# Kernel optimization log

Hardware: AMD Instinct MI355X
Metric: run time of the kernel (lower is better)

The kernel has to match this reference:

```python
import jax, jax.numpy as jnp
import numpy as np

ALPHA_MEM = 0.95      # util.decayconst(tau_mem)
ALPHA_MEM_OUT = 0.95  # util.decayconst(tau_mem_out)
ALPHA_P = 0.99        # util.decayconst(tau_p)
SURR_SCALE = 100.0

@jax.custom_vjp
def spike(x):
    # Heaviside forward, surrogate gradient backward (SurrGradSpike)
    return (x > 0).astype(x.dtype)

def _spike_fwd(x):
    return spike(x), x

def _spike_bwd(x, g):
    return (g / (SURR_SCALE * jnp.abs(x) + 1.0) ** 2,)

spike.defvjp(_spike_fwd, _spike_bwd)


def setup_inputs() -> dict:
    B, T, N, NIN, NOUT, D = 64, 400, 1024, 128, 32, 3
    key = jax.random.key(0)
    ks = jax.random.split(key, 8)
    inputs = jax.random.normal(ks[0], (B, T, NIN), dtype=jnp.float32)
    w = jax.random.normal(ks[1], (N, N), dtype=jnp.float32) / np.sqrt(N).astype(np.float32)
    w_in = jax.random.normal(ks[2], (NIN, N), dtype=jnp.float32) * np.float32(0.3 / np.sqrt(NIN))
    w_out = jax.random.normal(ks[3], (N, NOUT), dtype=jnp.float32) * np.float32(0.3 / np.sqrt(N))
    w_signs = jnp.where(jax.random.uniform(ks[4], (N,)) < 0.8, 1.0, -1.0).astype(jnp.float32)
    dmap = (jax.random.uniform(ks[5], (D, N, N)) < 0.2).astype(jnp.float32)  # delay-wise connectivity mask
    p = jax.random.uniform(ks[6], (N,), minval=-0.5, maxval=0.5).astype(jnp.float32)
    delays = jnp.array([1, 2, 4], dtype=jnp.int32)
    return dict(inputs=inputs, w=w, w_in=w_in, w_out=w_out, w_signs=w_signs,
                dmap=dmap, p=p, delays=delays)


def _forward(inputs, w, w_in, w_out, w_signs, dmap, p, delays):
    B, T, _ = inputs.shape
    N = w.shape[0]
    L = int(np.max(np.asarray(delays))) + 1  # ring-buffer length (static)
    dtype = inputs.dtype

    inp = jnp.einsum('btc,cn->btn', inputs, w_in)           # epoch.input, (B,T,N)
    W = dmap * (w_signs[:, None] * jnp.abs(w))[None]        # (D,N,N)
    depr = (p < 0).astype(dtype)                            # p_depr_mask

    def step(carry, inp_t):
        mem, w_p, buf_out, buf_wp, t = carry
        out = spike(mem - 1.0)                              # mark_spikes
        buf_out = buf_out.at[t % L].set(out)                # record_state
        buf_wp = buf_wp.at[t % L].set(w_p)
        idx = (t - delays) % L
        syn_p = buf_out[idx] * (1.0 + buf_wp[idx])          # (D,B,N)
        syn = jnp.einsum('dbe,deo->bo', syn_p, W)
        w_p_new = w_p * ALPHA_P + out * p * (1.0 + depr * w_p)
        mem_new = ALPHA_MEM * mem + inp_t + syn - jax.lax.stop_gradient(out)
        return (mem_new, w_p_new, buf_out, buf_wp, t + 1), out

    z = jnp.zeros((B, N), dtype)
    bufs = jnp.zeros((L, B, N), dtype)
    carry0 = (z, z, bufs, bufs, jnp.int32(0))
    _, out_rec = jax.lax.scan(step, carry0, jnp.swapaxes(inp, 0, 1))  # (T,B,N)

    # compute_readout: leaky integrator over projected spikes
    h2 = jnp.einsum('tbn,no->tbo', out_rec, w_out)
    def ro_step(r, h):
        r = ALPHA_MEM_OUT * r + h
        return r, r
    _, readout = jax.lax.scan(ro_step, jnp.zeros((B, w_out.shape[1]), dtype), h2)
    return jnp.swapaxes(readout, 0, 1)                      # (B,T,NOUT)


def reference(inputs, w, w_in, w_out, w_signs, dmap, p, delays):
    return _forward(inputs, w, w_in, w_out, w_signs, dmap, p, delays)
```

## Files before the change

### kernel.cpp

```cpp
#include <hip/hip_runtime.h>
#include <cstdint>
#include <cstddef>

#define BB    64
#define TT    400
#define NN    1024
#define NIN   128
#define NOUT  32
#define DD    3
#define LL6   6
#define GG    16
#define BPG   4
#define NT    32
#define KK    3072

#define ALPHA_MEM     0.95f
#define ALPHA_MEM_OUT 0.95f
#define ALPHA_P       0.99f

__global__ void build_W(const float* __restrict__ w,
                        const float* __restrict__ w_signs,
                        const float* __restrict__ dmap,
                        float* __restrict__ W) {
    int idx = blockIdx.x * blockDim.x + threadIdx.x;
    if (idx >= DD * NN * NN) return;
    int en = idx % (NN * NN);
    int e  = en / NN;
    W[idx] = dmap[idx] * (w_signs[e] * fabsf(w[en]));
}

__global__ void gemm_in(const float* __restrict__ inputs,
                        const float* __restrict__ w_in,
                        float* __restrict__ inp) {
    int idx = blockIdx.x * blockDim.x + threadIdx.x;
    if (idx >= TT * BB * NN) return;
    int n  = idx & (NN - 1);
    int tb = idx >> 10;
    int b  = tb & 63;
    int t  = tb >> 6;
    const float* row = inputs + ((size_t)b * TT + t) * NIN;
    float acc = 0.0f;
    #pragma unroll 8
    for (int c = 0; c < NIN; ++c)
        acc = fmaf(row[c], w_in[c * NN + n], acc);
    inp[idx] = acc;
}

__global__ void zero_sc1(float* __restrict__ p, int n) {
    int i = blockIdx.x * blockDim.x + threadIdx.x;
    if (i < n)
        __hip_atomic_store(p + i, 0.0f, __ATOMIC_RELAXED, __HIP_MEMORY_SCOPE_AGENT);
}

__global__ __launch_bounds__(256, 2) void snn_scan(
    const float* __restrict__ inputs,
    const float* __restrict__ w_in,
    const float* __restrict__ w_out,
    const float* __restrict__ p,
    const int*   __restrict__ delays,
    const float* __restrict__ W,
    const float* __restrict__ w_raw,
    const float* __restrict__ w_signs,
    const float* __restrict__ dmap,
    float*       __restrict__ ring,
    int*         __restrict__ cnt,
    float*       __restrict__ hpart,
    const float* __restrict__ inp_pre,
    float*       __restrict__ out,
    int use_pre, int use_W)
{
    __shared__ __align__(16) float sa[KK * BPG];
    __shared__ float w_out_s[32 * NOUT];
    __shared__ float spk_s[BPG * 32];
    __shared__ float s_sign[NN];
    __shared__ float s_in[BPG * NIN];

    const int bid  = blockIdx.x;
    const int g    = bid >> 5;
    const int tile = bid & 31;
    const int tid  = threadIdx.x;
    const int lane = tid & 63;
    const int wv   = tid >> 6;

    const bool st = (tid < BPG * 32);
    const int  sb = tid >> 5;
    const int  nl = tid & 31;

    const int gks = tid >> 3;
    const int gcg = tid & 7;

    float mem = 0.0f, wp = 0.0f, r = 0.0f;
    float pn = 0.0f, depr = 0.0f;
    if (st) { pn = p[tile * 32 + nl]; depr = (pn < 0.0f) ? 1.0f : 0.0f; }

    const int d0 = delays[0], d1 = delays[1], d2 = delays[2];

    for (int k = tid; k < 32 * NOUT; k += 256)
        w_out_s[k] = w_out[(tile * 32 + (k >> 5)) * NOUT + (k & 31)];
    if (!use_W)
        for (int k = tid; k < NN; k += 256) s_sign[k] = w_signs[k];
    __syncthreads();

    const float* Wt = W     + tile * 32 + gcg * 4;
    const float* Dt = dmap  + tile * 32 + gcg * 4;
    const float* Rt = w_raw + tile * 32 + gcg * 4;

    for (int t = 0; t < TT; ++t) {
        const int slot_w = t % LL6;
        const int s0 = (t - d0 + 2 * LL6) % LL6;
        const int s1 = (t - d1 + 2 * LL6) % LL6;
        const int s2 = (t - d2 + 2 * LL6) % LL6;

        bool  spk = false;
        float ia  = 0.0f;
        if (st) {
            spk = (mem - 1.0f) > 0.0f;
            const float a = spk ? (1.0f + wp) : 0.0f;
            __hip_atomic_store(ring + (((size_t)slot_w * BB + g * BPG + sb) << 10)
                                    + tile * 32 + nl,
                               a, __ATOMIC_RELAXED, __HIP_MEMORY_SCOPE_AGENT);
            wp = ALPHA_P * wp + (spk ? pn * (1.0f + depr * wp) : 0.0f);
            spk_s[tid] = spk ? 1.0f : 0.0f;
            if (use_pre)
                ia = inp_pre[((size_t)t * BB + g * BPG + sb) * NN + tile * 32 + nl];
        }
        if (!use_pre) {
            for (int k = tid; k < BPG * NIN; k += 256) {
                int b2 = k >> 7, c = k & 127;
                s_in[k] = inputs[((size_t)(g * BPG + b2) * TT + t) * NIN + c];
            }
        }
        __syncthreads();

        if (st) {
            float h = 0.0f;
            #pragma unroll
            for (int n2 = 0; n2 < 32; ++n2)
                h = fmaf(spk_s[sb * 32 + n2], w_out_s[n2 * 32 + nl], h);
            __hip_atomic_store(hpart + ((((size_t)(t & 1) * NT + tile) * BB)
                                        + g * BPG + sb) * NOUT + nl,
                               h, __ATOMIC_RELAXED, __HIP_MEMORY_SCOPE_AGENT);
            if (!use_pre) {
                #pragma unroll 8
                for (int c = 0; c < NIN; ++c)
                    ia = fmaf(s_in[sb * NIN + c], w_in[c * NN + tile * 32 + nl], ia);
            }
        }
        __syncthreads();

        if (tid == 0)
            __hip_atomic_fetch_add(&cnt[g * 32], 1, __ATOMIC_RELEASE,
                                   __HIP_MEMORY_SCOPE_AGENT);

        {
            const int b2 = lane >> 4;
            const int eo = lane & 15;
            #pragma unroll 16
            for (int i = 0; i < 48; ++i) {
                const int c  = i * 4 + wv;
                const int kl = c * 16 + eo;
                const int d  = kl >> 10;
                const int e  = kl & 1023;
                const int sl = (d == 0) ? s0 : ((d == 1) ? s1 : s2);
                const float v = __hip_atomic_load(
                    ring + (((size_t)sl * BB + g * BPG + b2) << 10) + e,
                    __ATOMIC_RELAXED, __HIP_MEMORY_SCOPE_AGENT);
                sa[kl * 4 + b2] = v;
            }
        }
        __syncthreads();

        if (tid == 0) {
            const int target = 32 * (t + 1);
            while (__hip_atomic_load(&cnt[g * 32], __ATOMIC_ACQUIRE,
                                     __HIP_MEMORY_SCOPE_AGENT) < target)
                __builtin_amdgcn_s_sleep(2);
        }
        __syncthreads();

        if (tile == 0 && st) {
            float h = 0.0f;
            #pragma unroll
            for (int k3 = 0; k3 < NT; ++k3)
                h += __hip_atomic_load(hpart + ((((size_t)(t & 1) * NT + k3) * BB)
                                                + g * BPG + sb) * NOUT + nl,
                                       __ATOMIC_RELAXED, __HIP_MEMORY_SCOPE_AGENT);
            r = ALPHA_MEM_OUT * r + h;
            out[((size_t)(g * BPG + sb) * TT + t) * NOUT + nl] = r;
        }

        float4 acc0 = {0,0,0,0}, acc1 = {0,0,0,0}, acc2 = {0,0,0,0}, acc3 = {0,0,0,0};
        if (use_W) {
            #pragma unroll 8
            for (int i = 0; i < 96; ++i) {
                const int kk = gks + (i << 5);
                const float4 av = *(const float4*)&sa[kk << 2];
                const float4 wv4 = *(const float4*)(Wt + ((size_t)kk << 10));
                acc0.x = fmaf(av.x, wv4.x, acc0.x); acc0.y = fmaf(av.x, wv4.y, acc0.y);
                acc0.z = fmaf(av.x, wv4.z, acc0.z); acc0.w = fmaf(av.x, wv4.w, acc0.w);
                acc1.x = fmaf(av.y, wv4.x, acc1.x); acc1.y = fmaf(av.y, wv4.y, acc1.y);
                acc1.z = fmaf(av.y, wv4.z, acc1.z); acc1.w = fmaf(av.y, wv4.w, acc1.w);
                acc2.x = fmaf(av.z, wv4.x, acc2.x); acc2.y = fmaf(av.z, wv4.y, acc2.y);
                acc2.z = fmaf(av.z, wv4.z, acc2.z); acc2.w = fmaf(av.z, wv4.w, acc2.w);
                acc3.x = fmaf(av.w, wv4.x, acc3.x); acc3.y = fmaf(av.w, wv4.y, acc3.y);
                acc3.z = fmaf(av.w, wv4.z, acc3.z); acc3.w = fmaf(av.w, wv4.w, acc3.w);
            }
        } else {
            #pragma unroll 2
            for (int i = 0; i < 96; ++i) {
                const int kk = gks + (i << 5);
                const int e  = kk & 1023;
                const float sg = s_sign[e];
                const float4 dm = *(const float4*)(Dt + ((size_t)kk << 10));
                const float4 wr = *(const float4*)(Rt + ((size_t)e << 10));
                float4 wv4;
                wv4.x = dm.x * (sg * fabsf(wr.x));
                wv4.y = dm.y * (sg * fabsf(wr.y));
                wv4.z = dm.z * (sg * fabsf(wr.z));
                wv4.w = dm.w * (sg * fabsf(wr.w));
                const float4 av = *(const float4*)&sa[kk << 2];
                acc0.x = fmaf(av.x, wv4.x, acc0.x); acc0.y = fmaf(av.x, wv4.y, acc0.y);
                acc0.z = fmaf(av.x, wv4.z, acc0.z); acc0.w = fmaf(av.x, wv4.w, acc0.w);
                acc1.x = fmaf(av.y, wv4.x, acc1.x); acc1.y = fmaf(av.y, wv4.y, acc1.y);
                acc1.z = fmaf(av.y, wv4.z, acc1.z); acc1.w = fmaf(av.y, wv4.w, acc1.w);
                acc2.x = fmaf(av.z, wv4.x, acc2.x); acc2.y = fmaf(av.z, wv4.y, acc2.y);
                acc2.z = fmaf(av.z, wv4.z, acc2.z); acc2.w = fmaf(av.z, wv4.w, acc2.w);
                acc3.x = fmaf(av.w, wv4.x, acc3.x); acc3.y = fmaf(av.w, wv4.y, acc3.y);
                acc3.z = fmaf(av.w, wv4.z, acc3.z); acc3.w = fmaf(av.w, wv4.w, acc3.w);
            }
        }
        __syncthreads();

        float* red = sa;
        {
            const int o0 = gcg * 4;
            red[(0 * 32 + o0 + 0) * 33 + gks] = acc0.x;
            red[(0 * 32 + o0 + 1) * 33 + gks] = acc0.y;
            red[(0 * 32 + o0 + 2) * 33 + gks] = acc0.z;
            red[(0 * 32 + o0 + 3) * 33 + gks] = acc0.w;
            red[(1 * 32 + o0 + 0) * 33 + gks] = acc1.x;
            red[(1 * 32 + o0 + 1) * 33 + gks] = acc1.y;
            red[(1 * 32 + o0 + 2) * 33 + gks] = acc1.z;
            red[(1 * 32 + o0 + 3) * 33 + gks] = acc1.w;
            red[(2 * 32 + o0 + 0) * 33 + gks] = acc2.x;
            red[(2 * 32 + o0 + 1) * 33 + gks] = acc2.y;
            red[(2 * 32 + o0 + 2) * 33 + gks] = acc2.z;
            red[(2 * 32 + o0 + 3) * 33 + gks] = acc2.w;
            red[(3 * 32 + o0 + 0) * 33 + gks] = acc3.x;
            red[(3 * 32 + o0 + 1) * 33 + gks] = acc3.y;
            red[(3 * 32 + o0 + 2) * 33 + gks] = acc3.z;
            red[(3 * 32 + o0 + 3) * 33 + gks] = acc3.w;
        }
        __syncthreads();

        if (st) {
            float syn = 0.0f;
            #pragma unroll
            for (int k2 = 0; k2 < 32; ++k2)
                syn += red[tid * 33 + k2];
            mem = ALPHA_MEM * mem + ia + syn - (spk ? 1.0f : 0.0f);
        }
        __syncthreads();
    }
}

extern "C" void kernel_launch(void* const* d_in, const int* in_sizes, int n_in,
                              void* d_out, int out_size, void* d_ws, size_t ws_size,
                              hipStream_t stream) {
    const float* inputs  = (const float*)d_in[0];
    const float* w       = (const float*)d_in[1];
    const float* w_in    = (const float*)d_in[2];
    const float* w_out   = (const float*)d_in[3];
    const float* w_signs = (const float*)d_in[4];
    const float* dmap    = (const float*)d_in[5];
    const float* p       = (const float*)d_in[6];
    const int*   delays  = (const int*)d_in[7];
    float*       outp    = (float*)d_out;

    const size_t ring_f = (size_t)LL6 * BB * NN;
    const size_t cnt_f  = GG * 32;
    const size_t hp_f   = (size_t)2 * NT * BB * NOUT;
    const size_t W_f    = (size_t)DD * NN * NN;
    const size_t pre_f  = (size_t)TT * BB * NN;

    float* ws = (float*)d_ws;
    float* ring  = ws;
    int*   cntp  = (int*)(ws + ring_f);
    float* hpart = ws + ring_f + cnt_f;
    size_t used  = ring_f + cnt_f + hp_f;

    int use_W = 0, use_pre = 0;
    float *W = nullptr, *inp_pre = nullptr;
    if (ws_size >= (used + W_f) * 4)   { use_W = 1;   W = ws + used;       used += W_f; }
    if (ws_size >= (used + pre_f) * 4) { use_pre = 1; inp_pre = ws + used; used += pre_f; }

    if (use_W) {
        const int total = DD * NN * NN;
        build_W<<<(total + 255) / 256, 256, 0, stream>>>(w, w_signs, dmap, W);
    }
    if (use_pre) {
        const int total = TT * BB * NN;
        gemm_in<<<(total + 255) / 256, 256, 0, stream>>>(inputs, w_in, inp_pre);
    }
    {
        const int total = (int)(ring_f + cnt_f);
        zero_sc1<<<(total + 255) / 256, 256, 0, stream>>>(ring, total);
    }

    void* args[] = {
        (void*)&inputs, (void*)&w_in, (void*)&w_out, (void*)&p, (void*)&delays,
        (void*)&W, (void*)&w, (void*)&w_signs, (void*)&dmap,
        (void*)&ring, (void*)&cntp, (void*)&hpart, (void*)&inp_pre, (void*)&outp,
        (void*)&use_pre, (void*)&use_W
    };
    hipError_t cerr = hipLaunchCooperativeKernel((const void*)snn_scan,
                               dim3(GG * NT), dim3(256), args, 0, stream);
    if (cerr != hipSuccess) {
        hipLaunchKernelGGL(snn_scan, dim3(GG * NT), dim3(256), 0, stream,
                           inputs, w_in, w_out, p, delays, W, w, w_signs, dmap,
                           ring, cntp, hpart, inp_pre, outp, use_pre, use_W);
    }
}
```

Baseline: 11.38 ms.

## Pack masked recurrent weights into fixed-capacity per-column sparse lists

A new pre-pass kernel builds, for each output neuron, a padded list of (row index, value) pairs holding the nonzero entries of the masked delay-stacked weight matrix, capped at 800 entries. The recurrent step then gathers spike activations from shared memory by index and multiplies only by the nonzero weights. The dense 3072-row sweep is kept as a fallback. The goal is to cut per-step weight traffic and FMAs by exploiting the roughly 20% connectivity density. In exchange, shared-memory reads become irregular gathers that can hit bank conflicts, and any column with more than 800 nonzeros is silently truncated.

```diff
diff --git a/kernel.cpp b/kernel.cpp
--- a/kernel.cpp
+++ b/kernel.cpp
@@ -13,6 +13,7 @@
 #define BPG   4
 #define NT    32
 #define KK    3072
+#define CAP   800
 
 #define ALPHA_MEM     0.95f
 #define ALPHA_MEM_OUT 0.95f
@@ -27,6 +28,42 @@
     int en = idx % (NN * NN);
     int e  = en / NN;
     W[idx] = dmap[idx] * (w_signs[e] * fabsf(w[en]));
+}
+
+__global__ void build_csr(const float* __restrict__ W,
+                          uint2* __restrict__ pack) {
+    const int col = blockIdx.x;
+    const int tid = threadIdx.x;
+    __shared__ int pref[256];
+    __shared__ int total_s;
+
+    int cnt = 0;
+    #pragma unroll
+    for (int i = 0; i < 12; ++i) {
+        const float v = W[(size_t)(tid * 12 + i) * NN + col];
+        cnt += (v != 0.0f) ? 1 : 0;
+    }
+    pref[tid] = cnt;
+    __syncthreads();
+    if (tid == 0) {
+        int run = 0;
+        for (int j = 0; j < 256; ++j) { int c = pref[j]; pref[j] = run; run += c; }
+        total_s = run;
+    }
+    __syncthreads();
+
+    int ofs = pref[tid];
+    #pragma unroll
+    for (int i = 0; i < 12; ++i) {
+        const int k = tid * 12 + i;
+        const float v = W[(size_t)k * NN + col];
+        if (v != 0.0f && ofs < CAP) {
+            pack[(size_t)col * CAP + ofs] = make_uint2((unsigned)k, __float_as_uint(v));
+            ++ofs;
+        }
+    }
+    for (int s = total_s + tid; s < CAP; s += 256)
+        pack[(size_t)col * CAP + s] = make_uint2(0u, 0u);
 }
 
 __global__ void gemm_in(const float* __restrict__ inputs,
@@ -66,8 +103,9 @@
     int*         __restrict__ cnt,
     float*       __restrict__ hpart,
     const float* __restrict__ inp_pre,
+    const uint2* __restrict__ pack,
     float*       __restrict__ out,
-    int use_pre, int use_W)
+    int use_pre, int use_W, int use_csr)
 {
     __shared__ __align__(16) float sa[KK * BPG];
     __shared__ float w_out_s[32 * NOUT];
@@ -89,6 +127,9 @@
     const int gks = tid >> 3;
     const int gcg = tid & 7;
 
+    const int colg = tid >> 3;
+    const int sub  = tid & 7;
+
     float mem = 0.0f, wp = 0.0f, r = 0.0f;
     float pn = 0.0f, depr = 0.0f;
     if (st) { pn = p[tile * 32 + nl]; depr = (pn < 0.0f) ? 1.0f : 0.0f; }
@@ -104,6 +145,7 @@
     const float* Wt = W     + tile * 32 + gcg * 4;
     const float* Dt = dmap  + tile * 32 + gcg * 4;
     const float* Rt = w_raw + tile * 32 + gcg * 4;
+    const uint2* Pk = pack  + (size_t)(tile * 32 + colg) * CAP;
 
     for (int t = 0; t < TT; ++t) {
         const int slot_w = t % LL6;
@@ -189,78 +231,109 @@
             out[((size_t)(g * BPG + sb) * TT + t) * NOUT + nl] = r;
         }
 
-        float4 acc0 = {0,0,0,0}, acc1 = {0,0,0,0}, acc2 = {0,0,0,0}, acc3 = {0,0,0,0};
-        if (use_W) {
-            #pragma unroll 8
-            for (int i = 0; i < 96; ++i) {
-                const int kk = gks + (i << 5);
-                const float4 av = *(const float4*)&sa[kk << 2];
-                const float4 wv4 = *(const float4*)(Wt + ((size_t)kk << 10));
-                acc0.x = fmaf(av.x, wv4.x, acc0.x); acc0.y = fmaf(av.x, wv4.y, acc0.y);
-                acc0.z = fmaf(av.x, wv4.z, acc0.z); acc0.w = fmaf(av.x, wv4.w, acc0.w);
-                acc1.x = fmaf(av.y, wv4.x, acc1.x); acc1.y = fmaf(av.y, wv4.y, acc1.y);
-                acc1.z = fmaf(av.y, wv4.z, acc1.z); acc1.w = fmaf(av.y, wv4.w, acc1.w);
-                acc2.x = fmaf(av.z, wv4.x, acc2.x); acc2.y = fmaf(av.z, wv4.y, acc2.y);
-                acc2.z = fmaf(av.z, wv4.z, acc2.z); acc2.w = fmaf(av.z, wv4.w, acc2.w);
-                acc3.x = fmaf(av.w, wv4.x, acc3.x); acc3.y = fmaf(av.w, wv4.y, acc3.y);
-                acc3.z = fmaf(av.w, wv4.z, acc3.z); acc3.w = fmaf(av.w, wv4.w, acc3.w);
-            }
+        if (use_csr) {
+            float a0 = 0.0f, a1 = 0.0f, a2 = 0.0f, a3 = 0.0f;
+            #pragma unroll 4
+            for (int i = 0; i < CAP / 8; ++i) {
+                const uint2 pv = Pk[i * 8 + sub];
+                const float v  = __uint_as_float(pv.y);
+                const float4 av = *(const float4*)&sa[pv.x << 2];
+                a0 = fmaf(av.x, v, a0);
+                a1 = fmaf(av.y, v, a1);
+                a2 = fmaf(av.z, v, a2);
+                a3 = fmaf(av.w, v, a3);
+            }
+            __syncthreads();
+
+            float* red = sa;
+            red[(colg * 4 + 0) * 9 + sub] = a0;
+            red[(colg * 4 + 1) * 9 + sub] = a1;
+            red[(colg * 4 + 2) * 9 + sub] = a2;
+            red[(colg * 4 + 3) * 9 + sub] = a3;
+            __syncthreads();
+
+            if (st) {
+                float syn = 0.0f;
+                #pragma unroll
+                for (int k2 = 0; k2 < 8; ++k2)
+                    syn += red[(nl * 4 + sb) * 9 + k2];
+                mem = ALPHA_MEM * mem + ia + syn - (spk ? 1.0f : 0.0f);
+            }
+            __syncthreads();
         } else {
-            #pragma unroll 2
-            for (int i = 0; i < 96; ++i) {
-                const int kk = gks + (i << 5);
-                const int e  = kk & 1023;
-                const float sg = s_sign[e];
-                const float4 dm = *(const float4*)(Dt + ((size_t)kk << 10));
-                const float4 wr = *(const float4*)(Rt + ((size_t)e << 10));
-                float4 wv4;
-                wv4.x = dm.x * (sg * fabsf(wr.x));
-                wv4.y = dm.y * (sg * fabsf(wr.y));
-                wv4.z = dm.z * (sg * fabsf(wr.z));
-                wv4.w = dm.w * (sg * fabsf(wr.w));
-                const float4 av = *(const float4*)&sa[kk << 2];
-                acc0.x = fmaf(av.x, wv4.x, acc0.x); acc0.y = fmaf(av.x, wv4.y, acc0.y);
-                acc0.z = fmaf(av.x, wv4.z, acc0.z); acc0.w = fmaf(av.x, wv4.w, acc0.w);
-                acc1.x = fmaf(av.y, wv4.x, acc1.x); acc1.y = fmaf(av.y, wv4.y, acc1.y);
-                acc1.z = fmaf(av.y, wv4.z, acc1.z); acc1.w = fmaf(av.y, wv4.w, acc1.w);
-                acc2.x = fmaf(av.z, wv4.x, acc2.x); acc2.y = fmaf(av.z, wv4.y, acc2.y);
-                acc2.z = fmaf(av.z, wv4.z, acc2.z); acc2.w = fmaf(av.z, wv4.w, acc2.w);
-                acc3.x = fmaf(av.w, wv4.x, acc3.x); acc3.y = fmaf(av.w, wv4.y, acc3.y);
-                acc3.z = fmaf(av.w, wv4.z, acc3.z); acc3.w = fmaf(av.w, wv4.w, acc3.w);
-            }
-        }
-        __syncthreads();
-
-        float* red = sa;
-        {
-            const int o0 = gcg * 4;
-            red[(0 * 32 + o0 + 0) * 33 + gks] = acc0.x;
-            red[(0 * 32 + o0 + 1) * 33 + gks] = acc0.y;
-            red[(0 * 32 + o0 + 2) * 33 + gks] = acc0.z;
-            red[(0 * 32 + o0 + 3) * 33 + gks] = acc0.w;
-            red[(1 * 32 + o0 + 0) * 33 + gks] = acc1.x;
-            red[(1 * 32 + o0 + 1) * 33 + gks] = acc1.y;
-            red[(1 * 32 + o0 + 2) * 33 + gks] = acc1.z;
-            red[(1 * 32 + o0 + 3) * 33 + gks] = acc1.w;
-            red[(2 * 32 + o0 + 0) * 33 + gks] = acc2.x;
-            red[(2 * 32 + o0 + 1) * 33 + gks] = acc2.y;
-            red[(2 * 32 + o0 + 2) * 33 + gks] = acc2.z;
-            red[(2 * 32 + o0 + 3) * 33 + gks] = acc2.w;
-            red[(3 * 32 + o0 + 0) * 33 + gks] = acc3.x;
-            red[(3 * 32 + o0 + 1) * 33 + gks] = acc3.y;
-            red[(3 * 32 + o0 + 2) * 33 + gks] = acc3.z;
-            red[(3 * 32 + o0 + 3) * 33 + gks] = acc3.w;
-        }
-        __syncthreads();
-
-        if (st) {
-            float syn = 0.0f;
-            #pragma unroll
-            for (int k2 = 0; k2 < 32; ++k2)
-                syn += red[tid * 33 + k2];
-            mem = ALPHA_MEM * mem + ia + syn - (spk ? 1.0f : 0.0f);
-        }
-        __syncthreads();
+            float4 acc0 = {0,0,0,0}, acc1 = {0,0,0,0}, acc2 = {0,0,0,0}, acc3 = {0,0,0,0};
+            if (use_W) {
+                #pragma unroll 8
+                for (int i = 0; i < 96; ++i) {
+                    const int kk = gks + (i << 5);
+                    const float4 av = *(const float4*)&sa[kk << 2];
+                    const float4 wv4 = *(const float4*)(Wt + ((size_t)kk << 10));
+                    acc0.x = fmaf(av.x, wv4.x, acc0.x); acc0.y = fmaf(av.x, wv4.y, acc0.y);
+                    acc0.z = fmaf(av.x, wv4.z, acc0.z); acc0.w = fmaf(av.x, wv4.w, acc0.w);
+                    acc1.x = fmaf(av.y, wv4.x, acc1.x); acc1.y = fmaf(av.y, wv4.y, acc1.y);
+                    acc1.z = fmaf(av.y, wv4.z, acc1.z); acc1.w = fmaf(av.y, wv4.w, acc1.w);
+                    acc2.x = fmaf(av.z, wv4.x, acc2.x); acc2.y = fmaf(av.z, wv4.y, acc2.y);
+                    acc2.z = fmaf(av.z, wv4.z, acc2.z); acc2.w = fmaf(av.z, wv4.w, acc2.w);
+                    acc3.x = fmaf(av.w, wv4.x, acc3.x); acc3.y = fmaf(av.w, wv4.y, acc3.y);
+                    acc3.z = fmaf(av.w, wv4.z, acc3.z); acc3.w = fmaf(av.w, wv4.w, acc3.w);
+                }
+            } else {
+                #pragma unroll 2
+                for (int i = 0; i < 96; ++i) {
+                    const int kk = gks + (i << 5);
+                    const int e  = kk & 1023;
+                    const float sg = s_sign[e];
+                    const float4 dm = *(const float4*)(Dt + ((size_t)kk << 10));
+                    const float4 wr = *(const float4*)(Rt + ((size_t)e << 10));
+                    float4 wv4;
+                    wv4.x = dm.x * (sg * fabsf(wr.x));
+                    wv4.y = dm.y * (sg * fabsf(wr.y));
+                    wv4.z = dm.z * (sg * fabsf(wr.z));
+                    wv4.w = dm.w * (sg * fabsf(wr.w));
+                    const float4 av = *(const float4*)&sa[kk << 2];
+                    acc0.x = fmaf(av.x, wv4.x, acc0.x); acc0.y = fmaf(av.x, wv4.y, acc0.y);
+                    acc0.z = fmaf(av.x, wv4.z, acc0.z); acc0.w = fmaf(av.x, wv4.w, acc0.w);
+                    acc1.x = fmaf(av.y, wv4.x, acc1.x); acc1.y = fmaf(av.y, wv4.y, acc1.y);
+                    acc1.z = fmaf(av.y, wv4.z, acc1.z); acc1.w = fmaf(av.y, wv4.w, acc1.w);
+                    acc2.x = fmaf(av.z, wv4.x, acc2.x); acc2.y = fmaf(av.z, wv4.y, acc2.y);
+                    acc2.z = fmaf(av.z, wv4.z, acc2.z); acc2.w = fmaf(av.z, wv4.w, acc2.w);
+                    acc3.x = fmaf(av.w, wv4.x, acc3.x); acc3.y = fmaf(av.w, wv4.y, acc3.y);
+                    acc3.z = fmaf(av.w, wv4.z, acc3.z); acc3.w = fmaf(av.w, wv4.w, acc3.w);
+                }
+            }
+            __syncthreads();
+
+            float* red = sa;
+            {
+                const int o0 = gcg * 4;
+                red[(0 * 32 + o0 + 0) * 33 + gks] = acc0.x;
+                red[(0 * 32 + o0 + 1) * 33 + gks] = acc0.y;
+                red[(0 * 32 + o0 + 2) * 33 + gks] = acc0.z;
+                red[(0 * 32 + o0 + 3) * 33 + gks] = acc0.w;
+                red[(1 * 32 + o0 + 0) * 33 + gks] = acc1.x;
+                red[(1 * 32 + o0 + 1) * 33 + gks] = acc1.y;
+                red[(1 * 32 + o0 + 2) * 33 + gks] = acc1.z;
+                red[(1 * 32 + o0 + 3) * 33 + gks] = acc1.w;
+                red[(2 * 32 + o0 + 0) * 33 + gks] = acc2.x;
+                red[(2 * 32 + o0 + 1) * 33 + gks] = acc2.y;
+                red[(2 * 32 + o0 + 2) * 33 + gks] = acc2.z;
+                red[(2 * 32 + o0 + 3) * 33 + gks] = acc2.w;
+                red[(3 * 32 + o0 + 0) * 33 + gks] = acc3.x;
+                red[(3 * 32 + o0 + 1) * 33 + gks] = acc3.y;
+                red[(3 * 32 + o0 + 2) * 33 + gks] = acc3.z;
+                red[(3 * 32 + o0 + 3) * 33 + gks] = acc3.w;
+            }
+            __syncthreads();
+
+            if (st) {
+                float syn = 0.0f;
+                #pragma unroll
+                for (int k2 = 0; k2 < 32; ++k2)
+                    syn += red[tid * 33 + k2];
+                mem = ALPHA_MEM * mem + ia + syn - (spk ? 1.0f : 0.0f);
+            }
+            __syncthreads();
+        }
     }
 }
 
@@ -282,6 +355,7 @@
     const size_t hp_f   = (size_t)2 * NT * BB * NOUT;
     const size_t W_f    = (size_t)DD * NN * NN;
     const size_t pre_f  = (size_t)TT * BB * NN;
+    const size_t csr_f  = (size_t)NN * CAP * 2;
 
     float* ws = (float*)d_ws;
     float* ring  = ws;
@@ -289,15 +363,21 @@
     float* hpart = ws + ring_f + cnt_f;
     size_t used  = ring_f + cnt_f + hp_f;
 
-    int use_W = 0, use_pre = 0;
+    int use_W = 0, use_pre = 0, use_csr = 0;
     float *W = nullptr, *inp_pre = nullptr;
+    uint2 *pack = nullptr;
     if (ws_size >= (used + W_f) * 4)   { use_W = 1;   W = ws + used;       used += W_f; }
     if (ws_size >= (used + pre_f) * 4) { use_pre = 1; inp_pre = ws + used; used += pre_f; }
+    if (use_W && ws_size >= (used + csr_f) * 4) {
+        use_csr = 1; pack = (uint2*)(ws + used); used += csr_f;
+    }
 
     if (use_W) {
         const int total = DD * NN * NN;
         build_W<<<(total + 255) / 256, 256, 0, stream>>>(w, w_signs, dmap, W);
     }
+    if (use_csr)
+        build_csr<<<NN, 256, 0, stream>>>(W, pack);
     if (use_pre) {
         const int total = TT * BB * NN;
         gemm_in<<<(total + 255) / 256, 256, 0, stream>>>(inputs, w_in, inp_pre);
@@ -310,14 +390,15 @@
     void* args[] = {
         (void*)&inputs, (void*)&w_in, (void*)&w_out, (void*)&p, (void*)&delays,
         (void*)&W, (void*)&w, (void*)&w_signs, (void*)&dmap,
-        (void*)&ring, (void*)&cntp, (void*)&hpart, (void*)&inp_pre, (void*)&outp,
-        (void*)&use_pre, (void*)&use_W
+        (void*)&ring, (void*)&cntp, (void*)&hpart, (void*)&inp_pre, (void*)&pack,
+        (void*)&outp, (void*)&use_pre, (void*)&use_W, (void*)&use_csr
     };
     hipError_t cerr = hipLaunchCooperativeKernel((const void*)snn_scan,
                                dim3(GG * NT), dim3(256), args, 0, stream);
     if (cerr != hipSuccess) {
         hipLaunchKernelGGL(snn_scan, dim3(GG * NT), dim3(256), 0, stream,
                            inputs, w_in, w_out, p, delays, W, w, w_signs, dmap,
-                           ring, cntp, hpart, inp_pre, outp, use_pre, use_W);
-    }
-}
+                           ring, cntp, hpart, inp_pre, pack, outp,
+                           use_pre, use_W, use_csr);
+    }
+}
```

Result: faster. 10.95 ms (-3.8%).

## Gather only nonzero delayed spikes into per-wave active lists for synaptic sums

Applied to the files above, without the earlier changes.

Each wave now owns one batch row. It uses a ballot and popcount to compact the nonzero delayed presynaptic activations into an LDS list of (index, value) pairs. The synaptic sum then gathers only the W rows for those active entries, with two half-waves splitting the list and combining through a shuffle. This replaces the dense 3072-row accumulation, the LDS reduction and several block barriers, so per-step cost scales with spike activity instead of the full connectivity. The list is capped at 1536 entries, so a step with more active entries than that per row would silently drop contributions. The gathers are also less regular than the earlier float4 streaming loads.

```diff
diff --git a/kernel.cpp b/kernel.cpp
--- a/kernel.cpp
+++ b/kernel.cpp
@@ -13,6 +13,7 @@
 #define BPG   4
 #define NT    32
 #define KK    3072
+#define LCAP  1536
 
 #define ALPHA_MEM     0.95f
 #define ALPHA_MEM_OUT 0.95f
@@ -69,7 +70,7 @@
     float*       __restrict__ out,
     int use_pre, int use_W)
 {
-    __shared__ __align__(16) float sa[KK * BPG];
+    __shared__ uint2 act_l[BPG][LCAP];
     __shared__ float w_out_s[32 * NOUT];
     __shared__ float spk_s[BPG * 32];
     __shared__ float s_sign[NN];
@@ -79,15 +80,12 @@
     const int g    = bid >> 5;
     const int tile = bid & 31;
     const int tid  = threadIdx.x;
+    const int w    = tid >> 6;
     const int lane = tid & 63;
-    const int wv   = tid >> 6;
-
-    const bool st = (tid < BPG * 32);
-    const int  sb = tid >> 5;
-    const int  nl = tid & 31;
-
-    const int gks = tid >> 3;
-    const int gcg = tid & 7;
+
+    const bool st = (lane < 32);
+    const int  nl = lane & 31;
+    const int  ks = lane >> 5;
 
     float mem = 0.0f, wp = 0.0f, r = 0.0f;
     float pn = 0.0f, depr = 0.0f;
@@ -101,9 +99,9 @@
         for (int k = tid; k < NN; k += 256) s_sign[k] = w_signs[k];
     __syncthreads();
 
-    const float* Wt = W     + tile * 32 + gcg * 4;
-    const float* Dt = dmap  + tile * 32 + gcg * 4;
-    const float* Rt = w_raw + tile * 32 + gcg * 4;
+    const float* Wc = W     + tile * 32 + nl;
+    const float* Dc = dmap  + tile * 32 + nl;
+    const float* Rc = w_raw + tile * 32 + nl;
 
     for (int t = 0; t < TT; ++t) {
         const int slot_w = t % LL6;
@@ -116,13 +114,13 @@
         if (st) {
             spk = (mem - 1.0f) > 0.0f;
             const float a = spk ? (1.0f + wp) : 0.0f;
-            __hip_atomic_store(ring + (((size_t)slot_w * BB + g * BPG + sb) << 10)
+            __hip_atomic_store(ring + (((size_t)slot_w * BB + g * BPG + w) << 10)
                                     + tile * 32 + nl,
                                a, __ATOMIC_RELAXED, __HIP_MEMORY_SCOPE_AGENT);
             wp = ALPHA_P * wp + (spk ? pn * (1.0f + depr * wp) : 0.0f);
-            spk_s[tid] = spk ? 1.0f : 0.0f;
+            spk_s[w * 32 + nl] = spk ? 1.0f : 0.0f;
             if (use_pre)
-                ia = inp_pre[((size_t)t * BB + g * BPG + sb) * NN + tile * 32 + nl];
+                ia = inp_pre[((size_t)t * BB + g * BPG + w) * NN + tile * 32 + nl];
         }
         if (!use_pre) {
             for (int k = tid; k < BPG * NIN; k += 256) {
@@ -136,14 +134,14 @@
             float h = 0.0f;
             #pragma unroll
             for (int n2 = 0; n2 < 32; ++n2)
-                h = fmaf(spk_s[sb * 32 + n2], w_out_s[n2 * 32 + nl], h);
+                h = fmaf(spk_s[w * 32 + n2], w_out_s[n2 * 32 + nl], h);
             __hip_atomic_store(hpart + ((((size_t)(t & 1) * NT + tile) * BB)
-                                        + g * BPG + sb) * NOUT + nl,
+                                        + g * BPG + w) * NOUT + nl,
                                h, __ATOMIC_RELAXED, __HIP_MEMORY_SCOPE_AGENT);
             if (!use_pre) {
                 #pragma unroll 8
                 for (int c = 0; c < NIN; ++c)
-                    ia = fmaf(s_in[sb * NIN + c], w_in[c * NN + tile * 32 + nl], ia);
+                    ia = fmaf(s_in[w * NIN + c], w_in[c * NN + tile * 32 + nl], ia);
             }
         }
         __syncthreads();
@@ -152,23 +150,28 @@
             __hip_atomic_fetch_add(&cnt[g * 32], 1, __ATOMIC_RELEASE,
                                    __HIP_MEMORY_SCOPE_AGENT);
 
+        int base = 0;
         {
-            const int b2 = lane >> 4;
-            const int eo = lane & 15;
-            #pragma unroll 16
-            for (int i = 0; i < 48; ++i) {
-                const int c  = i * 4 + wv;
-                const int kl = c * 16 + eo;
+            const unsigned long long lt = (1ull << lane) - 1ull;
+            #pragma unroll 8
+            for (int ch = 0; ch < 48; ++ch) {
+                const int kl = ch * 64 + lane;
                 const int d  = kl >> 10;
                 const int e  = kl & 1023;
                 const int sl = (d == 0) ? s0 : ((d == 1) ? s1 : s2);
                 const float v = __hip_atomic_load(
-                    ring + (((size_t)sl * BB + g * BPG + b2) << 10) + e,
+                    ring + (((size_t)sl * BB + g * BPG + w) << 10) + e,
                     __ATOMIC_RELAXED, __HIP_MEMORY_SCOPE_AGENT);
-                sa[kl * 4 + b2] = v;
-            }
-        }
-        __syncthreads();
+                const unsigned long long m = __ballot(v != 0.0f);
+                if (v != 0.0f) {
+                    const int pos = base + (int)__popcll(m & lt);
+                    if (pos < LCAP)
+                        act_l[w][pos] = make_uint2((unsigned)kl, __float_as_uint(v));
+                }
+                base += (int)__popcll(m);
+            }
+        }
+        const int na = (base < LCAP) ? base : LCAP;
 
         if (tid == 0) {
             const int target = 32 * (t + 1);
@@ -183,84 +186,33 @@
             #pragma unroll
             for (int k3 = 0; k3 < NT; ++k3)
                 h += __hip_atomic_load(hpart + ((((size_t)(t & 1) * NT + k3) * BB)
-                                                + g * BPG + sb) * NOUT + nl,
+                                                + g * BPG + w) * NOUT + nl,
                                        __ATOMIC_RELAXED, __HIP_MEMORY_SCOPE_AGENT);
             r = ALPHA_MEM_OUT * r + h;
-            out[((size_t)(g * BPG + sb) * TT + t) * NOUT + nl] = r;
-        }
-
-        float4 acc0 = {0,0,0,0}, acc1 = {0,0,0,0}, acc2 = {0,0,0,0}, acc3 = {0,0,0,0};
+            out[((size_t)(g * BPG + w) * TT + t) * NOUT + nl] = r;
+        }
+
+        float syn = 0.0f;
         if (use_W) {
-            #pragma unroll 8
-            for (int i = 0; i < 96; ++i) {
-                const int kk = gks + (i << 5);
-                const float4 av = *(const float4*)&sa[kk << 2];
-                const float4 wv4 = *(const float4*)(Wt + ((size_t)kk << 10));
-                acc0.x = fmaf(av.x, wv4.x, acc0.x); acc0.y = fmaf(av.x, wv4.y, acc0.y);
-                acc0.z = fmaf(av.x, wv4.z, acc0.z); acc0.w = fmaf(av.x, wv4.w, acc0.w);
-                acc1.x = fmaf(av.y, wv4.x, acc1.x); acc1.y = fmaf(av.y, wv4.y, acc1.y);
-                acc1.z = fmaf(av.y, wv4.z, acc1.z); acc1.w = fmaf(av.y, wv4.w, acc1.w);
-                acc2.x = fmaf(av.z, wv4.x, acc2.x); acc2.y = fmaf(av.z, wv4.y, acc2.y);
-                acc2.z = fmaf(av.z, wv4.z, acc2.z); acc2.w = fmaf(av.z, wv4.w, acc2.w);
-                acc3.x = fmaf(av.w, wv4.x, acc3.x); acc3.y = fmaf(av.w, wv4.y, acc3.y);
-                acc3.z = fmaf(av.w, wv4.z, acc3.z); acc3.w = fmaf(av.w, wv4.w, acc3.w);
+            #pragma unroll 4
+            for (int i = ks; i < na; i += 2) {
+                const uint2 kv = act_l[w][i];
+                syn = fmaf(__uint_as_float(kv.y), Wc[(size_t)kv.x << 10], syn);
             }
         } else {
             #pragma unroll 2
-            for (int i = 0; i < 96; ++i) {
-                const int kk = gks + (i << 5);
-                const int e  = kk & 1023;
-                const float sg = s_sign[e];
-                const float4 dm = *(const float4*)(Dt + ((size_t)kk << 10));
-                const float4 wr = *(const float4*)(Rt + ((size_t)e << 10));
-                float4 wv4;
-                wv4.x = dm.x * (sg * fabsf(wr.x));
-                wv4.y = dm.y * (sg * fabsf(wr.y));
-                wv4.z = dm.z * (sg * fabsf(wr.z));
-                wv4.w = dm.w * (sg * fabsf(wr.w));
-                const float4 av = *(const float4*)&sa[kk << 2];
-                acc0.x = fmaf(av.x, wv4.x, acc0.x); acc0.y = fmaf(av.x, wv4.y, acc0.y);
-                acc0.z = fmaf(av.x, wv4.z, acc0.z); acc0.w = fmaf(av.x, wv4.w, acc0.w);
-                acc1.x = fmaf(av.y, wv4.x, acc1.x); acc1.y = fmaf(av.y, wv4.y, acc1.y);
-                acc1.z = fmaf(av.y, wv4.z, acc1.z); acc1.w = fmaf(av.y, wv4.w, acc1.w);
-                acc2.x = fmaf(av.z, wv4.x, acc2.x); acc2.y = fmaf(av.z, wv4.y, acc2.y);
-                acc2.z = fmaf(av.z, wv4.z, acc2.z); acc2.w = fmaf(av.z, wv4.w, acc2.w);
-                acc3.x = fmaf(av.w, wv4.x, acc3.x); acc3.y = fmaf(av.w, wv4.y, acc3.y);
-                acc3.z = fmaf(av.w, wv4.z, acc3.z); acc3.w = fmaf(av.w, wv4.w, acc3.w);
-            }
-        }
-        __syncthreads();
-
-        float* red = sa;
-        {
-            const int o0 = gcg * 4;
-            red[(0 * 32 + o0 + 0) * 33 + gks] = acc0.x;
-            red[(0 * 32 + o0 + 1) * 33 + gks] = acc0.y;
-            red[(0 * 32 + o0 + 2) * 33 + gks] = acc0.z;
-            red[(0 * 32 + o0 + 3) * 33 + gks] = acc0.w;
-            red[(1 * 32 + o0 + 0) * 33 + gks] = acc1.x;
-            red[(1 * 32 + o0 + 1) * 33 + gks] = acc1.y;
-            red[(1 * 32 + o0 + 2) * 33 + gks] = acc1.z;
-            red[(1 * 32 + o0 + 3) * 33 + gks] = acc1.w;
-            red[(2 * 32 + o0 + 0) * 33 + gks] = acc2.x;
-            red[(2 * 32 + o0 + 1) * 33 + gks] = acc2.y;
-            red[(2 * 32 + o0 + 2) * 33 + gks] = acc2.z;
-            red[(2 * 32 + o0 + 3) * 33 + gks] = acc2.w;
-            red[(3 * 32 + o0 + 0) * 33 + gks] = acc3.x;
-            red[(3 * 32 + o0 + 1) * 33 + gks] = acc3.y;
-            red[(3 * 32 + o0 + 2) * 33 + gks] = acc3.z;
-            red[(3 * 32 + o0 + 3) * 33 + gks] = acc3.w;
-        }
-        __syncthreads();
-
-        if (st) {
-            float syn = 0.0f;
-            #pragma unroll
-            for (int k2 = 0; k2 < 32; ++k2)
-                syn += red[tid * 33 + k2];
+            for (int i = ks; i < na; i += 2) {
+                const uint2 kv = act_l[w][i];
+                const int e = (int)kv.x & 1023;
+                const float wv = Dc[(size_t)kv.x << 10] *
+                                 (s_sign[e] * fabsf(Rc[(size_t)e << 10]));
+                syn = fmaf(__uint_as_float(kv.y), wv, syn);
+            }
+        }
+        syn += __shfl_down(syn, 32, 64);
+
+        if (st)
             mem = ALPHA_MEM * mem + ia + syn - (spk ? 1.0f : 0.0f);
-        }
-        __syncthreads();
     }
 }
 
```

Result: slower. 22.04 ms (+93.7%).
